# Kernel tuning notes

Hardware: AMD Instinct MI355X
Metric: run time of the kernel (lower is better)

## Reference

```python
import jax, jax.numpy as jnp
import numpy as np

# dims: batch, samples, agents, obs_dim, action_dim, hidden
B, S, N, D, A, H = 512, 64, 8, 64, 16, 256
IN_DIM = (D + A) * N  # 640


def mish(x):
    return x * jnp.tanh(jax.nn.softplus(x))


def setup_inputs() -> dict:
    key = jax.random.key(0)
    ks = jax.random.split(key, 9)
    u = lambda k, shape, fan_in: jax.random.uniform(
        k, shape, jnp.float32, -1.0 / np.sqrt(fan_in), 1.0 / np.sqrt(fan_in))
    return {
        "state": jax.random.normal(ks[0], (B, N, D), jnp.float32),
        "action": jax.random.normal(ks[1], (B, N, A), jnp.float32),
        "W1": u(ks[2], (IN_DIM, H), IN_DIM),
        "b1": u(ks[3], (H,), IN_DIM),
        "W2": u(ks[4], (H, H), H),
        "b2": u(ks[5], (H,), H),
        "W3": u(ks[6], (H, 1), H),
        "b3": u(ks[7], (1,), H),
        # random grand-coalition permutations of the N agents, per (batch, sample)
        "perm": jnp.argsort(jax.random.uniform(ks[8], (B, S, N)), axis=-1).astype(jnp.int32),
    }


def reference(state, action, W1, b1, W2, b2, W3, b3, perm):
    # subcoalition mask [B,S,N,N]: torch builds one-hot(perm) @ tril(ones),
    # i.e. mask[b,s,i,j] = 1 iff j <= perm[b,s,i]
    subcoal = (jnp.arange(N) <= perm[..., None]).astype(state.dtype)
    # gathered actions in coalition order [B,S,N,A]: act_g[b,s,j] = action[b, perm[b,s,j]]
    act_g = action[jnp.arange(B)[:, None, None], perm]
    # masked subcoalition actions [B,S,N,N,A] -> [B,S,N,N*A]
    act = (act_g[:, :, None, :, :] * subcoal[..., None]).reshape(B, S, N, N * A)
    # flattened global obs broadcast over (sample, agent) axes [B,S,N,N*D]
    obs = jnp.broadcast_to(state.reshape(B, 1, 1, N * D), (B, S, N, N * D))
    x = jnp.concatenate([obs, act], axis=-1)  # [B,S,N,IN_DIM]
    # per-agent loop in torch uses shared q1 weights -> single batched MLP
    h = mish(x @ W1 + b1)
    h = mish(h @ W2 + b2)
    q = h @ W3 + b3                   # [B,S,N,1]
    q1 = q.mean(axis=1).squeeze(-1)   # mean over samples -> [B,N]
    return (q1, q1)
```

## Files before the change

kernel.cpp:

```cpp
#include <hip/hip_runtime.h>

typedef unsigned short ushort_t;
typedef _Float16 half_t;
typedef __attribute__((ext_vector_type(2))) _Float16 half2_t;
typedef __attribute__((ext_vector_type(8))) _Float16 half8_t;
typedef __attribute__((ext_vector_type(2))) __fp16 fp16x2;
typedef __attribute__((ext_vector_type(2))) float fx2;
typedef __attribute__((ext_vector_type(4))) float floatx4;

#define LOG2E 1.4426950408889634f
#define LN2   0.6931471805599453f

__device__ __forceinline__ float exp2_(float x) {
#if __has_builtin(__builtin_amdgcn_exp2f)
    return __builtin_amdgcn_exp2f(x);
#else
    return exp2f(x);
#endif
}

__device__ __forceinline__ half2_t cvt_pk_f16(float a, float b) {
    auto r = __builtin_amdgcn_cvt_pkrtz(a, b);
    return __builtin_bit_cast(half2_t, r);
}

__device__ __forceinline__ float fdot2_(half2_t a, half2_t b) {
#if __has_builtin(__builtin_amdgcn_fdot2)
    return __builtin_amdgcn_fdot2(__builtin_bit_cast(fp16x2, a),
                                  __builtin_bit_cast(fp16x2, b), 0.0f, false);
#else
    return (float)a.x * (float)b.x + (float)a.y * (float)b.y;
#endif
}

__device__ __forceinline__ fx2 mish2(fx2 t0) {
    fx2 one = {1.0f, 1.0f};
    fx2 m2  = {-2.0f, -2.0f};
    fx2 u   = {exp2_(t0.x), exp2_(t0.y)};
    fx2 s   = u + one;
    fx2 wv  = __builtin_elementwise_fma(s, s, one);
    fx2 rr  = {__builtin_amdgcn_rcpf(wv.x), __builtin_amdgcn_rcpf(wv.y)};
    fx2 v   = __builtin_elementwise_fma(rr, m2, one);
    return t0 * v;
}

__device__ __forceinline__ float dpp_sum16(float v) {
    int x = __float_as_int(v);
    v += __int_as_float(__builtin_amdgcn_update_dpp(0, x, 0xB1, 0xF, 0xF, true));
    x = __float_as_int(v);
    v += __int_as_float(__builtin_amdgcn_update_dpp(0, x, 0x4E, 0xF, 0xF, true));
    x = __float_as_int(v);
    v += __int_as_float(__builtin_amdgcn_update_dpp(0, x, 0x124, 0xF, 0xF, true));
    x = __float_as_int(v);
    v += __int_as_float(__builtin_amdgcn_update_dpp(0, x, 0x128, 0xF, 0xF, true));
    return v;
}

__global__ __launch_bounds__(256) void prep_kernel(
        const float* __restrict__ state,
        const float* __restrict__ action,
        const float* __restrict__ W1,
        const float* __restrict__ W2,
        float* __restrict__ obsWp,
        half_t* __restrict__ actW,
        half_t* __restrict__ W2T,
        float* __restrict__ out) {
    int bid = blockIdx.x;
    int t = threadIdx.x;
    if (bid < 512) {
        int bg = bid >> 3;
        int kc = bid & 7;
        int bs = bg * 8;
        const float* w1p = W1 + (size_t)(kc * 64) * 256 + t;
        const float* stp = state + (size_t)bs * 512 + kc * 64;
        float acc[8];
#pragma unroll
        for (int bb = 0; bb < 8; ++bb) acc[bb] = 0.f;
#pragma unroll 4
        for (int f = 0; f < 64; ++f) {
            float w = w1p[f * 256];
#pragma unroll
            for (int bb = 0; bb < 8; ++bb)
                acc[bb] = fmaf(stp[bb * 512 + f], w, acc[bb]);
        }
#pragma unroll
        for (int bb = 0; bb < 8; ++bb)
            obsWp[(size_t)kc * 131072 + (bs + bb) * 256 + t] = acc[bb];
    } else if (bid < 1536) {
        int idx = bid - 512;
        int j = idx & 7;
        int b0 = (idx >> 3) * 4;
        const float* W1a = W1 + (size_t)(512 + j * 16) * 256;
        float wv[16];
#pragma unroll
        for (int a = 0; a < 16; ++a) wv[a] = W1a[a * 256 + t];
#pragma unroll
        for (int bb = 0; bb < 4; ++bb) {
            int b = b0 + bb;
            const float* acp = action + (size_t)b * 128;
            float acc[8];
#pragma unroll
            for (int n = 0; n < 8; ++n) acc[n] = 0.f;
#pragma unroll
            for (int a = 0; a < 16; ++a) {
#pragma unroll
                for (int n = 0; n < 8; ++n)
                    acc[n] = fmaf(acp[n * 16 + a], wv[a], acc[n]);
            }
#pragma unroll
            for (int n = 0; n < 8; ++n)
                actW[(((size_t)b * 8 + n) * 8 + j) * 256 + t] = (half_t)(acc[n] * LOG2E);
        }
    } else {
        int blk = bid - 1536;
        if (blk < 16) {
            out[blk * 512 + t] = 0.0f;
            out[blk * 512 + 256 + t] = 0.0f;
        }
        int n = blk * 8 + (t >> 5);
        int klo = t & 31;
#pragma unroll
        for (int kk = 0; kk < 8; ++kk) {
            int k = kk * 32 + klo;
            W2T[n * 256 + k] = (half_t)W2[k * 256 + n];
        }
    }
}

#define CHUNK_US 528

__global__ __launch_bounds__(512, 4) void main_kernel(
        const float* __restrict__ obsWp, const half_t* __restrict__ actW,
        const half_t* __restrict__ W2T, const int* __restrict__ perm,
        const float* __restrict__ b1, const float* __restrict__ b2,
        const float* __restrict__ W3, const float* __restrict__ b3,
        float* __restrict__ out) {
    __shared__ __align__(16) ushort_t h1[2][32 * CHUNK_US];
    __shared__ __align__(16) float obsb[256];
    __shared__ int perm_s[128];
    __shared__ float qpart[2][8][64];

    int t = threadIdx.x;
    int bid = blockIdx.x;
    int b = (bid & 7) * 64 + ((bid >> 3) & 63);
    int sgp = bid >> 9;
    int s0 = sgp * 16;

    int w = t >> 6;
    int L = t & 63;
    int lo = L & 15;
    int q = L >> 4;

    const half_t* w2base = W2T + ((size_t)(w * 32 + lo)) * 256 + q * 8;
    half8_t bpre[4];
    bpre[0] = *reinterpret_cast<const half8_t*>(w2base + 0 * 4096 + 0 * 32);
    bpre[1] = *reinterpret_cast<const half8_t*>(w2base + 1 * 4096 + 0 * 32);
    bpre[2] = *reinterpret_cast<const half8_t*>(w2base + 0 * 4096 + 1 * 32);
    bpre[3] = *reinterpret_cast<const half8_t*>(w2base + 1 * 4096 + 1 * 32);

    int col0 = w * 32 + lo;
    int col1 = col0 + 16;
    fx2 b2p = {b2[col0] * LOG2E, b2[col1] * LOG2E};
    half2_t w3p = cvt_pk_f16(W3[col0] * LN2, W3[col1] * LN2);

    const int* prow = perm + ((size_t)b * 64 + s0 + w) * 8;
    int4 pa0 = *reinterpret_cast<const int4*>(prow);
    int4 pa1 = *reinterpret_cast<const int4*>(prow + 4);
    int4 pb0 = *reinterpret_cast<const int4*>(prow + 64);
    int4 pb1 = *reinterpret_cast<const int4*>(prow + 68);

    if (t < 256) {
        float s = b1[t];
#pragma unroll
        for (int c = 0; c < 8; ++c) s += obsWp[(size_t)c * 131072 + b * 256 + t];
        obsb[t] = s * LOG2E;
    } else if (t < 384) {
        perm_s[t - 256] = perm[((size_t)b * 64 + s0) * 8 + (t - 256)];
    }

    int g = L >> 1;
    int ksg = g >> 2;
    int qq = g & 3;
    int halfsel = L & 1;
    const half_t* actg = actW + (size_t)b * 64 * 256 + L * 4;
    int dstoff = qq * 128 + halfsel * 4 + ksg * CHUNK_US;

    int pj0[8] = {pa0.x, pa0.y, pa0.z, pa0.w, pa1.x, pa1.y, pa1.z, pa1.w};
    uint2 av0[8];
#pragma unroll
    for (int j = 0; j < 8; ++j)
        av0[j] = *reinterpret_cast<const uint2*>(actg + (pj0[j] * 8 + j) * 256);

    int phys = (q << 4) | ((lo + q) & 15);

    __syncthreads();

    float4 ob = *reinterpret_cast<const float4*>(obsb + L * 4);

    {
        fx2 r01 = {ob.x, ob.y};
        fx2 r23 = {ob.z, ob.w};
        ushort_t* dst0 = h1[0] + dstoff;
#pragma unroll
        for (int j = 0; j < 8; ++j) {
            half2_t a0 = __builtin_bit_cast(half2_t, av0[j].x);
            half2_t a1 = __builtin_bit_cast(half2_t, av0[j].y);
            r01 += (fx2){(float)a0.x, (float)a0.y};
            r23 += (fx2){(float)a1.x, (float)a1.y};
            fx2 h01 = mish2(r01);
            fx2 h23 = mish2(r23);
            int row = w * 8 + j;
            int mt2 = row >> 4, lr = row & 15;
            int lrs = (lr + qq) & 15;
            uint2 pk = make_uint2(__builtin_bit_cast(unsigned, cvt_pk_f16(h01.x, h01.y)),
                                  __builtin_bit_cast(unsigned, cvt_pk_f16(h23.x, h23.y)));
            *reinterpret_cast<uint2*>(dst0 + mt2 * 8 * CHUNK_US + lrs * 8) = pk;
        }
    }

    int pj1[8] = {pb0.x, pb0.y, pb0.z, pb0.w, pb1.x, pb1.y, pb1.z, pb1.w};
    uint2 av1[8];
#pragma unroll
    for (int j = 0; j < 8; ++j)
        av1[j] = *reinterpret_cast<const uint2*>(actg + (pj1[j] * 8 + j) * 256);

    __syncthreads();

    floatx4 acc0[4][2];
#pragma unroll
    for (int mt = 0; mt < 4; ++mt)
#pragma unroll
        for (int nt = 0; nt < 2; ++nt) acc0[mt][nt] = (floatx4){0.f, 0.f, 0.f, 0.f};
    {
        fx2 r01 = {ob.x, ob.y};
        fx2 r23 = {ob.z, ob.w};
        ushort_t* dst1 = h1[1] + dstoff;
        const ushort_t* h1b0 = h1[0] + phys * 8;
#pragma unroll
        for (int ks = 0; ks < 8; ++ks) {
            half8_t afr[4];
#pragma unroll
            for (int mt = 0; mt < 4; ++mt)
                afr[mt] = *reinterpret_cast<const half8_t*>(h1b0 + (mt * 8 + ks) * CHUNK_US);
            half8_t bfr0 = (ks == 0) ? bpre[0] : (ks == 1) ? bpre[2]
                         : *reinterpret_cast<const half8_t*>(w2base + 0 * 4096 + ks * 32);
            half8_t bfr1 = (ks == 0) ? bpre[1] : (ks == 1) ? bpre[3]
                         : *reinterpret_cast<const half8_t*>(w2base + 1 * 4096 + ks * 32);
#pragma unroll
            for (int mt = 0; mt < 4; ++mt) {
                acc0[mt][0] = __builtin_amdgcn_mfma_f32_16x16x32_f16(afr[mt], bfr0, acc0[mt][0], 0, 0, 0);
                acc0[mt][1] = __builtin_amdgcn_mfma_f32_16x16x32_f16(afr[mt], bfr1, acc0[mt][1], 0, 0, 0);
            }
            {
                half2_t a0 = __builtin_bit_cast(half2_t, av1[ks].x);
                half2_t a1 = __builtin_bit_cast(half2_t, av1[ks].y);
                r01 += (fx2){(float)a0.x, (float)a0.y};
                r23 += (fx2){(float)a1.x, (float)a1.y};
                fx2 h01 = mish2(r01);
                fx2 h23 = mish2(r23);
                int row = w * 8 + ks;
                int mt2 = row >> 4, lr = row & 15;
                int lrs = (lr + qq) & 15;
                uint2 pk = make_uint2(__builtin_bit_cast(unsigned, cvt_pk_f16(h01.x, h01.y)),
                                      __builtin_bit_cast(unsigned, cvt_pk_f16(h23.x, h23.y)));
                *reinterpret_cast<uint2*>(dst1 + mt2 * 8 * CHUNK_US + lrs * 8) = pk;
            }
        }
    }
    __syncthreads();

    floatx4 acc1[4][2];
#pragma unroll
    for (int mt = 0; mt < 4; ++mt)
#pragma unroll
        for (int nt = 0; nt < 2; ++nt) acc1[mt][nt] = (floatx4){0.f, 0.f, 0.f, 0.f};
    {
        const ushort_t* h1b1 = h1[1] + phys * 8;
#pragma unroll
        for (int ks = 0; ks < 8; ++ks) {
            half8_t afr[4];
#pragma unroll
            for (int mt = 0; mt < 4; ++mt)
                afr[mt] = *reinterpret_cast<const half8_t*>(h1b1 + (mt * 8 + ks) * CHUNK_US);
            half8_t bfr0 = (ks == 0) ? bpre[0] : (ks == 1) ? bpre[2]
                         : *reinterpret_cast<const half8_t*>(w2base + 0 * 4096 + ks * 32);
            half8_t bfr1 = (ks == 0) ? bpre[1] : (ks == 1) ? bpre[3]
                         : *reinterpret_cast<const half8_t*>(w2base + 1 * 4096 + ks * 32);
#pragma unroll
            for (int mt = 0; mt < 4; ++mt) {
                acc1[mt][0] = __builtin_amdgcn_mfma_f32_16x16x32_f16(afr[mt], bfr0, acc1[mt][0], 0, 0, 0);
                acc1[mt][1] = __builtin_amdgcn_mfma_f32_16x16x32_f16(afr[mt], bfr1, acc1[mt][1], 0, 0, 0);
            }
#pragma unroll
            for (int v = 0; v < 2; ++v) {
                int idx = ks * 2 + v;
                int mt = idx >> 2, r = idx & 3;
                fx2 t2 = {acc0[mt][0][r], acc0[mt][1][r]};
                t2 += b2p;
                fx2 hh = mish2(t2);
                float part = fdot2_(cvt_pk_f16(hh.x, hh.y), w3p);
                float s = dpp_sum16(part);
                if (lo == 0) qpart[0][w][mt * 16 + q * 4 + r] = s;
            }
        }
    }
#pragma unroll
    for (int idx = 0; idx < 16; ++idx) {
        int mt = idx >> 2, r = idx & 3;
        fx2 t2 = {acc1[mt][0][r], acc1[mt][1][r]};
        t2 += b2p;
        fx2 hh = mish2(t2);
        float part = fdot2_(cvt_pk_f16(hh.x, hh.y), w3p);
        float s = dpp_sum16(part);
        if (lo == 0) qpart[1][w][mt * 16 + q * 4 + r] = s;
    }
    __syncthreads();

    if (t < 16) {
        int h = t >> 3, i = t & 7;
        float p = 0.f;
#pragma unroll
        for (int sl = 0; sl < 8; ++sl) {
            int k = perm_s[(h * 8 + sl) * 8 + i];
            int row = sl * 8 + k;
            float qv = b3[0];
#pragma unroll
            for (int ww = 0; ww < 8; ++ww) qv += qpart[h][ww][row];
            p += qv;
        }
        p *= (1.0f / 64.0f);
        atomicAdd(&out[b * 8 + i], p);
        atomicAdd(&out[4096 + b * 8 + i], p);
    }
}

extern "C" void kernel_launch(void* const* d_in, const int* in_sizes, int n_in,
                              void* d_out, int out_size, void* d_ws, size_t ws_size,
                              hipStream_t stream) {
    const float* state  = (const float*)d_in[0];
    const float* action = (const float*)d_in[1];
    const float* W1     = (const float*)d_in[2];
    const float* b1     = (const float*)d_in[3];
    const float* W2     = (const float*)d_in[4];
    const float* b2     = (const float*)d_in[5];
    const float* W3     = (const float*)d_in[6];
    const float* b3     = (const float*)d_in[7];
    const int*   perm   = (const int*)d_in[8];
    float* out = (float*)d_out;

    char* ws = (char*)d_ws;
    float*  obsWp = (float*)ws;
    half_t* actW  = (half_t*)(ws + 4194304);
    half_t* W2T   = (half_t*)(ws + 4194304 + 16777216);

    prep_kernel<<<1568, 256, 0, stream>>>(state, action, W1, W2, obsWp, actW, W2T, out);
    main_kernel<<<2048, 512, 0, stream>>>(obsWp, actW, W2T, perm, b1, b2, W3, b3, out);
}
```

Before: 164.2 us.

## Process four sample groups per block with a software-pipelined double buffer

```diff
diff --git a/kernel.cpp b/kernel.cpp
--- a/kernel.cpp
+++ b/kernel.cpp
@@ -129,6 +129,64 @@
 
 #define CHUNK_US 528
 
+template<bool EP, bool BUILD>
+__device__ __forceinline__ void kphase(
+        const ushort_t* __restrict__ rd, const half_t* __restrict__ w2base,
+        const half8_t* bpre,
+        floatx4 (&acc)[4][2], floatx4 (&accp)[4][2],
+        float* qbase, fx2 b2p, half2_t w3p, int w, int lo, int q,
+        const uint2* av, float4 ob, ushort_t* dst, int qq) {
+#pragma unroll
+    for (int mt = 0; mt < 4; ++mt)
+#pragma unroll
+        for (int nt = 0; nt < 2; ++nt) acc[mt][nt] = (floatx4){0.f, 0.f, 0.f, 0.f};
+    fx2 r01 = {ob.x, ob.y};
+    fx2 r23 = {ob.z, ob.w};
+#pragma unroll
+    for (int ks = 0; ks < 8; ++ks) {
+        half8_t afr[4];
+#pragma unroll
+        for (int mt = 0; mt < 4; ++mt)
+            afr[mt] = *reinterpret_cast<const half8_t*>(rd + (mt * 8 + ks) * CHUNK_US);
+        half8_t bfr0 = (ks == 0) ? bpre[0] : (ks == 1) ? bpre[2]
+                     : *reinterpret_cast<const half8_t*>(w2base + 0 * 4096 + ks * 32);
+        half8_t bfr1 = (ks == 0) ? bpre[1] : (ks == 1) ? bpre[3]
+                     : *reinterpret_cast<const half8_t*>(w2base + 1 * 4096 + ks * 32);
+#pragma unroll
+        for (int mt = 0; mt < 4; ++mt) {
+            acc[mt][0] = __builtin_amdgcn_mfma_f32_16x16x32_f16(afr[mt], bfr0, acc[mt][0], 0, 0, 0);
+            acc[mt][1] = __builtin_amdgcn_mfma_f32_16x16x32_f16(afr[mt], bfr1, acc[mt][1], 0, 0, 0);
+        }
+        if (BUILD) {
+            half2_t a0 = __builtin_bit_cast(half2_t, av[ks].x);
+            half2_t a1 = __builtin_bit_cast(half2_t, av[ks].y);
+            r01 += (fx2){(float)a0.x, (float)a0.y};
+            r23 += (fx2){(float)a1.x, (float)a1.y};
+            fx2 h01 = mish2(r01);
+            fx2 h23 = mish2(r23);
+            int row = w * 8 + ks;
+            int mt2 = row >> 4, lr = row & 15;
+            int lrs = (lr + qq) & 15;
+            uint2 pk = make_uint2(__builtin_bit_cast(unsigned, cvt_pk_f16(h01.x, h01.y)),
+                                  __builtin_bit_cast(unsigned, cvt_pk_f16(h23.x, h23.y)));
+            *reinterpret_cast<uint2*>(dst + mt2 * 8 * CHUNK_US + lrs * 8) = pk;
+        }
+        if (EP) {
+#pragma unroll
+            for (int v = 0; v < 2; ++v) {
+                int idx = ks * 2 + v;
+                int mt = idx >> 2, r = idx & 3;
+                fx2 t2 = {accp[mt][0][r], accp[mt][1][r]};
+                t2 += b2p;
+                fx2 hh = mish2(t2);
+                float part = fdot2_(cvt_pk_f16(hh.x, hh.y), w3p);
+                float s = dpp_sum16(part);
+                if (lo == 0) qbase[w * 64 + mt * 16 + q * 4 + r] = s;
+            }
+        }
+    }
+}
+
 __global__ __launch_bounds__(512, 4) void main_kernel(
         const float* __restrict__ obsWp, const half_t* __restrict__ actW,
         const half_t* __restrict__ W2T, const int* __restrict__ perm,
@@ -137,14 +195,14 @@
         float* __restrict__ out) {
     __shared__ __align__(16) ushort_t h1[2][32 * CHUNK_US];
     __shared__ __align__(16) float obsb[256];
-    __shared__ int perm_s[128];
-    __shared__ float qpart[2][8][64];
+    __shared__ int perm_s[256];
+    __shared__ float qpart[4][8][64];
 
     int t = threadIdx.x;
     int bid = blockIdx.x;
     int b = (bid & 7) * 64 + ((bid >> 3) & 63);
     int sgp = bid >> 9;
-    int s0 = sgp * 16;
+    int s0 = sgp * 32;
 
     int w = t >> 6;
     int L = t & 63;
@@ -166,15 +224,13 @@
     const int* prow = perm + ((size_t)b * 64 + s0 + w) * 8;
     int4 pa0 = *reinterpret_cast<const int4*>(prow);
     int4 pa1 = *reinterpret_cast<const int4*>(prow + 4);
-    int4 pb0 = *reinterpret_cast<const int4*>(prow + 64);
-    int4 pb1 = *reinterpret_cast<const int4*>(prow + 68);
 
     if (t < 256) {
         float s = b1[t];
 #pragma unroll
         for (int c = 0; c < 8; ++c) s += obsWp[(size_t)c * 131072 + b * 256 + t];
         obsb[t] = s * LOG2E;
-    } else if (t < 384) {
+    } else {
         perm_s[t - 256] = perm[((size_t)b * 64 + s0) * 8 + (t - 256)];
     }
 
@@ -186,12 +242,16 @@
     int dstoff = qq * 128 + halfsel * 4 + ksg * CHUNK_US;
 
     int pj0[8] = {pa0.x, pa0.y, pa0.z, pa0.w, pa1.x, pa1.y, pa1.z, pa1.w};
-    uint2 av0[8];
+    uint2 av_a[8];
 #pragma unroll
     for (int j = 0; j < 8; ++j)
-        av0[j] = *reinterpret_cast<const uint2*>(actg + (pj0[j] * 8 + j) * 256);
+        av_a[j] = *reinterpret_cast<const uint2*>(actg + (pj0[j] * 8 + j) * 256);
 
     int phys = (q << 4) | ((lo + q) & 15);
+    ushort_t* dst0 = h1[0] + dstoff;
+    ushort_t* dst1 = h1[1] + dstoff;
+    const ushort_t* rd0 = h1[0] + phys * 8;
+    const ushort_t* rd1 = h1[1] + phys * 8;
 
     __syncthreads();
 
@@ -200,11 +260,10 @@
     {
         fx2 r01 = {ob.x, ob.y};
         fx2 r23 = {ob.z, ob.w};
-        ushort_t* dst0 = h1[0] + dstoff;
 #pragma unroll
         for (int j = 0; j < 8; ++j) {
-            half2_t a0 = __builtin_bit_cast(half2_t, av0[j].x);
-            half2_t a1 = __builtin_bit_cast(half2_t, av0[j].y);
+            half2_t a0 = __builtin_bit_cast(half2_t, av_a[j].x);
+            half2_t a1 = __builtin_bit_cast(half2_t, av_a[j].y);
             r01 += (fx2){(float)a0.x, (float)a0.y};
             r23 += (fx2){(float)a1.x, (float)a1.y};
             fx2 h01 = mish2(r01);
@@ -218,105 +277,64 @@
         }
     }
 
-    int pj1[8] = {pb0.x, pb0.y, pb0.z, pb0.w, pb1.x, pb1.y, pb1.z, pb1.w};
-    uint2 av1[8];
-#pragma unroll
-    for (int j = 0; j < 8; ++j)
-        av1[j] = *reinterpret_cast<const uint2*>(actg + (pj1[j] * 8 + j) * 256);
-
-    __syncthreads();
-
-    floatx4 acc0[4][2];
-#pragma unroll
-    for (int mt = 0; mt < 4; ++mt)
-#pragma unroll
-        for (int nt = 0; nt < 2; ++nt) acc0[mt][nt] = (floatx4){0.f, 0.f, 0.f, 0.f};
-    {
-        fx2 r01 = {ob.x, ob.y};
-        fx2 r23 = {ob.z, ob.w};
-        ushort_t* dst1 = h1[1] + dstoff;
-        const ushort_t* h1b0 = h1[0] + phys * 8;
-#pragma unroll
-        for (int ks = 0; ks < 8; ++ks) {
-            half8_t afr[4];
-#pragma unroll
-            for (int mt = 0; mt < 4; ++mt)
-                afr[mt] = *reinterpret_cast<const half8_t*>(h1b0 + (mt * 8 + ks) * CHUNK_US);
-            half8_t bfr0 = (ks == 0) ? bpre[0] : (ks == 1) ? bpre[2]
-                         : *reinterpret_cast<const half8_t*>(w2base + 0 * 4096 + ks * 32);
-            half8_t bfr1 = (ks == 0) ? bpre[1] : (ks == 1) ? bpre[3]
-                         : *reinterpret_cast<const half8_t*>(w2base + 1 * 4096 + ks * 32);
-#pragma unroll
-            for (int mt = 0; mt < 4; ++mt) {
-                acc0[mt][0] = __builtin_amdgcn_mfma_f32_16x16x32_f16(afr[mt], bfr0, acc0[mt][0], 0, 0, 0);
-                acc0[mt][1] = __builtin_amdgcn_mfma_f32_16x16x32_f16(afr[mt], bfr1, acc0[mt][1], 0, 0, 0);
-            }
-            {
-                half2_t a0 = __builtin_bit_cast(half2_t, av1[ks].x);
-                half2_t a1 = __builtin_bit_cast(half2_t, av1[ks].y);
-                r01 += (fx2){(float)a0.x, (float)a0.y};
-                r23 += (fx2){(float)a1.x, (float)a1.y};
-                fx2 h01 = mish2(r01);
-                fx2 h23 = mish2(r23);
-                int row = w * 8 + ks;
-                int mt2 = row >> 4, lr = row & 15;
-                int lrs = (lr + qq) & 15;
-                uint2 pk = make_uint2(__builtin_bit_cast(unsigned, cvt_pk_f16(h01.x, h01.y)),
-                                      __builtin_bit_cast(unsigned, cvt_pk_f16(h23.x, h23.y)));
-                *reinterpret_cast<uint2*>(dst1 + mt2 * 8 * CHUNK_US + lrs * 8) = pk;
-            }
-        }
-    }
-    __syncthreads();
-
-    floatx4 acc1[4][2];
-#pragma unroll
-    for (int mt = 0; mt < 4; ++mt)
-#pragma unroll
-        for (int nt = 0; nt < 2; ++nt) acc1[mt][nt] = (floatx4){0.f, 0.f, 0.f, 0.f};
-    {
-        const ushort_t* h1b1 = h1[1] + phys * 8;
-#pragma unroll
-        for (int ks = 0; ks < 8; ++ks) {
-            half8_t afr[4];
-#pragma unroll
-            for (int mt = 0; mt < 4; ++mt)
-                afr[mt] = *reinterpret_cast<const half8_t*>(h1b1 + (mt * 8 + ks) * CHUNK_US);
-            half8_t bfr0 = (ks == 0) ? bpre[0] : (ks == 1) ? bpre[2]
-                         : *reinterpret_cast<const half8_t*>(w2base + 0 * 4096 + ks * 32);
-            half8_t bfr1 = (ks == 0) ? bpre[1] : (ks == 1) ? bpre[3]
-                         : *reinterpret_cast<const half8_t*>(w2base + 1 * 4096 + ks * 32);
-#pragma unroll
-            for (int mt = 0; mt < 4; ++mt) {
-                acc1[mt][0] = __builtin_amdgcn_mfma_f32_16x16x32_f16(afr[mt], bfr0, acc1[mt][0], 0, 0, 0);
-                acc1[mt][1] = __builtin_amdgcn_mfma_f32_16x16x32_f16(afr[mt], bfr1, acc1[mt][1], 0, 0, 0);
-            }
-#pragma unroll
-            for (int v = 0; v < 2; ++v) {
-                int idx = ks * 2 + v;
-                int mt = idx >> 2, r = idx & 3;
-                fx2 t2 = {acc0[mt][0][r], acc0[mt][1][r]};
-                t2 += b2p;
-                fx2 hh = mish2(t2);
-                float part = fdot2_(cvt_pk_f16(hh.x, hh.y), w3p);
-                float s = dpp_sum16(part);
-                if (lo == 0) qpart[0][w][mt * 16 + q * 4 + r] = s;
-            }
-        }
-    }
+    uint2 av_b[8];
+#pragma unroll
+    for (int j = 0; j < 8; ++j) {
+        int p = perm_s[(1 * 8 + w) * 8 + j];
+        av_b[j] = *reinterpret_cast<const uint2*>(actg + (p * 8 + j) * 256);
+    }
+
+    __syncthreads();
+
+    floatx4 acc_a[4][2], acc_b[4][2];
+
+    kphase<false, true>(rd0, w2base, bpre, acc_a, acc_a,
+                        &qpart[0][0][0], b2p, w3p, w, lo, q,
+                        av_b, ob, dst1, qq);
+
+#pragma unroll
+    for (int j = 0; j < 8; ++j) {
+        int p = perm_s[(2 * 8 + w) * 8 + j];
+        av_a[j] = *reinterpret_cast<const uint2*>(actg + (p * 8 + j) * 256);
+    }
+
+    __syncthreads();
+
+    kphase<true, true>(rd1, w2base, bpre, acc_b, acc_a,
+                       &qpart[0][0][0], b2p, w3p, w, lo, q,
+                       av_a, ob, dst0, qq);
+
+#pragma unroll
+    for (int j = 0; j < 8; ++j) {
+        int p = perm_s[(3 * 8 + w) * 8 + j];
+        av_b[j] = *reinterpret_cast<const uint2*>(actg + (p * 8 + j) * 256);
+    }
+
+    __syncthreads();
+
+    kphase<true, true>(rd0, w2base, bpre, acc_a, acc_b,
+                       &qpart[1][0][0], b2p, w3p, w, lo, q,
+                       av_b, ob, dst1, qq);
+
+    __syncthreads();
+
+    kphase<true, false>(rd1, w2base, bpre, acc_b, acc_a,
+                        &qpart[2][0][0], b2p, w3p, w, lo, q,
+                        av_b, ob, dst1, qq);
+
 #pragma unroll
     for (int idx = 0; idx < 16; ++idx) {
         int mt = idx >> 2, r = idx & 3;
-        fx2 t2 = {acc1[mt][0][r], acc1[mt][1][r]};
+        fx2 t2 = {acc_b[mt][0][r], acc_b[mt][1][r]};
         t2 += b2p;
         fx2 hh = mish2(t2);
         float part = fdot2_(cvt_pk_f16(hh.x, hh.y), w3p);
         float s = dpp_sum16(part);
-        if (lo == 0) qpart[1][w][mt * 16 + q * 4 + r] = s;
-    }
-    __syncthreads();
-
-    if (t < 16) {
+        if (lo == 0) qpart[3][w][mt * 16 + q * 4 + r] = s;
+    }
+    __syncthreads();
+
+    if (t < 32) {
         int h = t >> 3, i = t & 7;
         float p = 0.f;
 #pragma unroll
@@ -354,5 +372,5 @@
     half_t* W2T   = (half_t*)(ws + 4194304 + 16777216);
 
     prep_kernel<<<1568, 256, 0, stream>>>(state, action, W1, W2, obsWp, actW, W2T, out);
-    main_kernel<<<2048, 512, 0, stream>>>(obsWp, actW, W2T, perm, b1, b2, W3, b3, out);
-}
+    main_kernel<<<1024, 512, 0, stream>>>(obsWp, actW, W2T, perm, b1, b2, W3, b3, out);
+}
```

Result: slower. 185.9 us (+13.2%).
